# Optimization experiments

Measured on AMD Instinct MI355X. Metric: run time of the kernel, lower is better.

Reference implementation:

```python
import jax, jax.numpy as jnp
import numpy as np

N_EDGES = 320000
HIDDEN = 128
EDGE_DIM = 8


def setup_inputs() -> dict:
    key = jax.random.key(0)
    k1, k2, k3, k4 = jax.random.split(key, 4)
    h_v = jax.random.normal(k1, (N_EDGES, HIDDEN), dtype=jnp.float32)
    h_w = jax.random.normal(k2, (N_EDGES, HIDDEN), dtype=jnp.float32)
    # discrete edge types, one-hot encoded as float (as the module expects)
    edge_types = jax.random.randint(k3, (N_EDGES,), 0, EDGE_DIM)
    edge_features = jax.nn.one_hot(edge_types, EDGE_DIM, dtype=jnp.float32)
    # learned parameter: one (hidden, hidden) matrix per edge type
    edge_matrices = jax.random.normal(k4, (EDGE_DIM, HIDDEN, HIDDEN), dtype=jnp.float32) * 0.01
    return {"h_v": h_v, "h_w": h_w, "edge_features": edge_features,
            "edge_matrices": edge_matrices}


def reference(h_v, h_w, edge_features, edge_matrices):
    # Torch: A = einsum('ek,khd->ehd', edge_features, edge_matrices)  (huge E,H,H)
    #        messages = bmm(A, h_w[..., None]).squeeze(-1)
    # Same math, fused to avoid the (E,H,H) intermediate:
    # per-type matvec: y_ekh = sum_d edge_matrices[k,h,d] * h_w[e,d]
    y = jnp.einsum('ed,khd->ekh', h_w, edge_matrices)   # (E, K, H)
    # select/mix by (one-hot) edge type
    messages = jnp.einsum('ek,ekh->eh', edge_features, y)  # (E, H)
    return messages
```

## Files before the change

### kernel.cpp

```cpp
#include <hip/hip_runtime.h>
#include <hip/hip_bf16.h>


#define NEDGES 320000
#define HIDDEN 128
#define CHUNK  512

typedef __bf16 bf16x8 __attribute__((ext_vector_type(8)));
typedef float  f32x4  __attribute__((ext_vector_type(4)));

__device__ inline bf16x8 pack8(const float4 v0, const float4 v1) {
    bf16x8 p;
    p[0] = (__bf16)v0.x; p[1] = (__bf16)v0.y; p[2] = (__bf16)v0.z; p[3] = (__bf16)v0.w;
    p[4] = (__bf16)v1.x; p[5] = (__bf16)v1.y; p[6] = (__bf16)v1.z; p[7] = (__bf16)v1.w;
    return p;
}

__global__ __launch_bounds__(256, 2) void matrix_message_kernel(
    const float* __restrict__ h_w,
    const float* __restrict__ ef,
    const float* __restrict__ M,
    float*       __restrict__ out)
{
    __shared__ unsigned short list[CHUNK];
    __shared__ int cnt;
    __shared__ __align__(16) unsigned char Abuf[64 * 272];

    const int tid  = threadIdx.x;
    const int w    = tid >> 6;
    const int lane = tid & 63;
    const int q    = lane >> 4;
    const int c    = lane & 15;
    const int k    = blockIdx.y;
    const int e0   = blockIdx.x * CHUNK;

    if (tid == 0) cnt = 0;

    const float* Mb = M + (size_t)k * (HIDDEN * HIDDEN);
    bf16x8 b[2][4];
#pragma unroll
    for (int nt = 0; nt < 2; ++nt)
#pragma unroll
        for (int kk = 0; kk < 4; ++kk) {
            const int h = 32 * w + nt * 16 + c;
            const float4* s4 = (const float4*)(Mb + (size_t)h * HIDDEN + kk * 32 + q * 8);
            b[nt][kk] = pack8(s4[0], s4[1]);
        }

    __syncthreads();

#pragma unroll
    for (int t = tid; t < CHUNK; t += 256) {
        float f = ef[(size_t)(e0 + t) * 8 + k];
        if (f > 0.5f) {
            int p = atomicAdd(&cnt, 1);
            list[p] = (unsigned short)t;
        }
    }
    __syncthreads();

    const int n_g = cnt;
    for (int g = 0; g < n_g; g += 64) {
#pragma unroll
        for (int r4 = 0; r4 < 4; ++r4) {
            const int r   = r4 * 16 + (tid >> 4);
            const int idx = g + r;
            const int e_loc = list[(idx < n_g) ? idx : 0];
            const float4* src = (const float4*)(h_w + (size_t)(e0 + e_loc) * HIDDEN);
            float4 v0 = src[(tid & 15) * 2];
            float4 v1 = src[(tid & 15) * 2 + 1];
            *(bf16x8*)(Abuf + r * 272 + (tid & 15) * 16) = pack8(v0, v1);
        }
        __syncthreads();

        for (int s = 0; s < 4 && g + s * 16 < n_g; ++s) {
            bf16x8 a[4];
#pragma unroll
            for (int kk = 0; kk < 4; ++kk)
                a[kk] = *(const bf16x8*)(Abuf + (s * 16 + c) * 272 + kk * 64 + q * 16);

            f32x4 acc0 = {0.f, 0.f, 0.f, 0.f};
            f32x4 acc1 = {0.f, 0.f, 0.f, 0.f};
#pragma unroll
            for (int kk = 0; kk < 4; ++kk) {
                acc0 = __builtin_amdgcn_mfma_f32_16x16x32_bf16(a[kk], b[0][kk], acc0, 0, 0, 0);
                acc1 = __builtin_amdgcn_mfma_f32_16x16x32_bf16(a[kk], b[1][kk], acc1, 0, 0, 0);
            }

#pragma unroll
            for (int reg = 0; reg < 4; ++reg) {
                const int idx = g + s * 16 + q * 4 + reg;
                if (idx < n_g) {
                    const size_t row = (size_t)(e0 + list[idx]) * HIDDEN;
                    out[row + 32 * w + c]      = acc0[reg];
                    out[row + 32 * w + 16 + c] = acc1[reg];
                }
            }
        }
        __syncthreads();
    }
}

extern "C" void kernel_launch(void* const* d_in, const int* in_sizes, int n_in,
                              void* d_out, int out_size, void* d_ws, size_t ws_size,
                              hipStream_t stream) {
    const float* h_w = (const float*)d_in[1];
    const float* ef  = (const float*)d_in[2];
    const float* M   = (const float*)d_in[3];
    float*       out = (float*)d_out;

    dim3 grid(NEDGES / CHUNK, 8, 1);
    dim3 block(256, 1, 1);
    matrix_message_kernel<<<grid, block, 0, stream>>>(h_w, ef, M, out);
}
```

Measured before the change: 370.0 us.

## Double-buffer gathered rows, ballot-compact edge lists, and vectorize output stores

Each block now covers a larger edge chunk. The gathered h_w tile is double-buffered in LDS, with the global loads for the next 64-row group issued into registers before the MFMAs on the current group, so gather latency overlaps compute and one barrier per iteration is dropped. Edge-list compaction uses a wave ballot plus popcount with one atomic per wave instead of one per matching edge. The MFMA operands are swapped so each lane holds four consecutive hidden outputs and can write them as float4 stores. Launch bounds request higher occupancy, which risks register pressure from the prefetch registers, and larger chunks mean fewer blocks.

```diff
diff --git a/kernel.cpp b/kernel.cpp
--- a/kernel.cpp
+++ b/kernel.cpp
@@ -4,7 +4,9 @@
 
 #define NEDGES 320000
 #define HIDDEN 128
-#define CHUNK  512
+#define CHUNK  2560
+#define RSTRIDE 272
+#define HALF   (64 * RSTRIDE)
 
 typedef __bf16 bf16x8 __attribute__((ext_vector_type(8)));
 typedef float  f32x4  __attribute__((ext_vector_type(4)));
@@ -16,7 +18,7 @@
     return p;
 }
 
-__global__ __launch_bounds__(256, 2) void matrix_message_kernel(
+__global__ __launch_bounds__(256, 4) void matrix_message_kernel(
     const float* __restrict__ h_w,
     const float* __restrict__ ef,
     const float* __restrict__ M,
@@ -24,7 +26,7 @@
 {
     __shared__ unsigned short list[CHUNK];
     __shared__ int cnt;
-    __shared__ __align__(16) unsigned char Abuf[64 * 272];
+    __shared__ __align__(16) unsigned char Abuf[2][HALF];
 
     const int tid  = threadIdx.x;
     const int w    = tid >> 6;
@@ -50,54 +52,85 @@
     __syncthreads();
 
 #pragma unroll
-    for (int t = tid; t < CHUNK; t += 256) {
-        float f = ef[(size_t)(e0 + t) * 8 + k];
-        if (f > 0.5f) {
-            int p = atomicAdd(&cnt, 1);
-            list[p] = (unsigned short)t;
+    for (int t0 = 0; t0 < CHUNK; t0 += 256) {
+        const int t = t0 + tid;
+        const bool m = ef[(size_t)(e0 + t) * 8 + k] > 0.5f;
+        const unsigned long long mask = __ballot(m);
+        int base = 0;
+        if (lane == 0) base = atomicAdd(&cnt, __popcll(mask));
+        base = __shfl(base, 0);
+        if (m) {
+            const int off = __popcll(mask & ((1ull << lane) - 1ull));
+            list[base + off] = (unsigned short)t;
         }
     }
     __syncthreads();
 
     const int n_g = cnt;
+    if (n_g == 0) return;
+
+    const int rr = tid >> 4;
+    const int cc = tid & 15;
+
+    float4 p0[4], p1[4];
+#pragma unroll
+    for (int r4 = 0; r4 < 4; ++r4) {
+        const int idx = r4 * 16 + rr;
+        const int e_loc = list[(idx < n_g) ? idx : 0];
+        const float4* src = (const float4*)(h_w + (size_t)(e0 + e_loc) * HIDDEN + cc * 8);
+        p0[r4] = src[0];
+        p1[r4] = src[1];
+    }
+#pragma unroll
+    for (int r4 = 0; r4 < 4; ++r4)
+        *(bf16x8*)(&Abuf[0][(r4 * 16 + rr) * RSTRIDE + cc * 16]) = pack8(p0[r4], p1[r4]);
+
+    int cur = 0;
     for (int g = 0; g < n_g; g += 64) {
-#pragma unroll
-        for (int r4 = 0; r4 < 4; ++r4) {
-            const int r   = r4 * 16 + (tid >> 4);
-            const int idx = g + r;
-            const int e_loc = list[(idx < n_g) ? idx : 0];
-            const float4* src = (const float4*)(h_w + (size_t)(e0 + e_loc) * HIDDEN);
-            float4 v0 = src[(tid & 15) * 2];
-            float4 v1 = src[(tid & 15) * 2 + 1];
-            *(bf16x8*)(Abuf + r * 272 + (tid & 15) * 16) = pack8(v0, v1);
-        }
         __syncthreads();
 
+        const bool pf = (g + 64 < n_g);
+        if (pf) {
+#pragma unroll
+            for (int r4 = 0; r4 < 4; ++r4) {
+                const int idx = g + 64 + r4 * 16 + rr;
+                const int e_loc = list[(idx < n_g) ? idx : 0];
+                const float4* src = (const float4*)(h_w + (size_t)(e0 + e_loc) * HIDDEN + cc * 8);
+                p0[r4] = src[0];
+                p1[r4] = src[1];
+            }
+        }
+
+        const unsigned char* Ab = Abuf[cur];
         for (int s = 0; s < 4 && g + s * 16 < n_g; ++s) {
             bf16x8 a[4];
 #pragma unroll
             for (int kk = 0; kk < 4; ++kk)
-                a[kk] = *(const bf16x8*)(Abuf + (s * 16 + c) * 272 + kk * 64 + q * 16);
+                a[kk] = *(const bf16x8*)(Ab + (s * 16 + c) * RSTRIDE + kk * 64 + q * 16);
 
             f32x4 acc0 = {0.f, 0.f, 0.f, 0.f};
             f32x4 acc1 = {0.f, 0.f, 0.f, 0.f};
 #pragma unroll
             for (int kk = 0; kk < 4; ++kk) {
-                acc0 = __builtin_amdgcn_mfma_f32_16x16x32_bf16(a[kk], b[0][kk], acc0, 0, 0, 0);
-                acc1 = __builtin_amdgcn_mfma_f32_16x16x32_bf16(a[kk], b[1][kk], acc1, 0, 0, 0);
+                acc0 = __builtin_amdgcn_mfma_f32_16x16x32_bf16(b[0][kk], a[kk], acc0, 0, 0, 0);
+                acc1 = __builtin_amdgcn_mfma_f32_16x16x32_bf16(b[1][kk], a[kk], acc1, 0, 0, 0);
             }
 
-#pragma unroll
-            for (int reg = 0; reg < 4; ++reg) {
-                const int idx = g + s * 16 + q * 4 + reg;
-                if (idx < n_g) {
-                    const size_t row = (size_t)(e0 + list[idx]) * HIDDEN;
-                    out[row + 32 * w + c]      = acc0[reg];
-                    out[row + 32 * w + 16 + c] = acc1[reg];
-                }
+            const int idx = g + s * 16 + c;
+            if (idx < n_g) {
+                float* dst = out + (size_t)(e0 + list[idx]) * HIDDEN + 32 * w + q * 4;
+                *(float4*)dst        = *(const float4*)&acc0;
+                *(float4*)(dst + 16) = *(const float4*)&acc1;
             }
         }
-        __syncthreads();
+
+        if (pf) {
+            unsigned char* An = Abuf[cur ^ 1];
+#pragma unroll
+            for (int r4 = 0; r4 < 4; ++r4)
+                *(bf16x8*)(&An[(r4 * 16 + rr) * RSTRIDE + cc * 16]) = pack8(p0[r4], p1[r4]);
+        }
+        cur ^= 1;
     }
 }
 
```

New measurement: 369.5 us. About the same (-0.1%).

## Stage type matrix in LDS, swap MFMA operands, register double-buffer edge gathers

Applied to the files above, without the earlier changes.

The per-type weight matrix is now converted to bf16 once per block and kept in LDS, and the MFMA operands are swapped so each wave holds 16 gathered edge rows in registers and loops over all 128 output columns. Each wave works on its own 16-edge groups with a two-stage register double buffer that prefetches the next group's gather while computing the current one, which removes the per-group __syncthreads. Stores become float4 per row, list compaction uses a wave ballot with one atomic per wave, and the chunk size grows to 2560 with launch bounds of 4 blocks per SU. This adds per-block LDS weight staging (about 34KB) and fewer blocks in the grid, and register pressure from the two 32-float buffers may limit occupancy.

```diff
diff --git a/kernel.cpp b/kernel.cpp
--- a/kernel.cpp
+++ b/kernel.cpp
@@ -4,10 +4,13 @@
 
 #define NEDGES 320000
 #define HIDDEN 128
-#define CHUNK  512
+#define CHUNK  2560
+#define RS     272
 
 typedef __bf16 bf16x8 __attribute__((ext_vector_type(8)));
 typedef float  f32x4  __attribute__((ext_vector_type(4)));
+
+struct G { float4 v[8]; };
 
 __device__ inline bf16x8 pack8(const float4 v0, const float4 v1) {
     bf16x8 p;
@@ -16,7 +19,48 @@
     return p;
 }
 
-__global__ __launch_bounds__(256, 2) void matrix_message_kernel(
+__device__ inline void gather(const float* __restrict__ h_w,
+                              const unsigned short* list, int e0, int n_g,
+                              int base, int q, int c, G& g) {
+    int idx = base + c;
+    if (idx >= n_g) idx = n_g - 1;
+    const float* src = h_w + (size_t)(e0 + list[idx]) * HIDDEN + q * 8;
+#pragma unroll
+    for (int kk = 0; kk < 4; ++kk) {
+        g.v[2 * kk]     = *(const float4*)(src + kk * 32);
+        g.v[2 * kk + 1] = *(const float4*)(src + kk * 32 + 4);
+    }
+}
+
+__device__ inline void compute(const unsigned char* Mlds,
+                               const unsigned short* list,
+                               float* __restrict__ out, int e0, int n_g,
+                               int base, int q, int c, const G& g) {
+    bf16x8 bf[4];
+#pragma unroll
+    for (int kk = 0; kk < 4; ++kk) bf[kk] = pack8(g.v[2 * kk], g.v[2 * kk + 1]);
+
+    const int  idx = base + c;
+    const bool ok  = idx < n_g;
+    float* dst = out + (size_t)(e0 + list[ok ? idx : 0]) * HIDDEN + q * 4;
+
+#pragma unroll
+    for (int nt = 0; nt < 8; ++nt) {
+        const unsigned char* arow = Mlds + (size_t)(nt * 16 + c) * RS + q * 16;
+        bf16x8 a0 = *(const bf16x8*)(arow);
+        bf16x8 a1 = *(const bf16x8*)(arow + 64);
+        bf16x8 a2 = *(const bf16x8*)(arow + 128);
+        bf16x8 a3 = *(const bf16x8*)(arow + 192);
+        f32x4 acc = {0.f, 0.f, 0.f, 0.f};
+        acc = __builtin_amdgcn_mfma_f32_16x16x32_bf16(a0, bf[0], acc, 0, 0, 0);
+        acc = __builtin_amdgcn_mfma_f32_16x16x32_bf16(a1, bf[1], acc, 0, 0, 0);
+        acc = __builtin_amdgcn_mfma_f32_16x16x32_bf16(a2, bf[2], acc, 0, 0, 0);
+        acc = __builtin_amdgcn_mfma_f32_16x16x32_bf16(a3, bf[3], acc, 0, 0, 0);
+        if (ok) *(float4*)(dst + nt * 16) = *(const float4*)&acc;
+    }
+}
+
+__global__ __launch_bounds__(256, 4) void matrix_message_kernel(
     const float* __restrict__ h_w,
     const float* __restrict__ ef,
     const float* __restrict__ M,
@@ -24,7 +68,7 @@
 {
     __shared__ unsigned short list[CHUNK];
     __shared__ int cnt;
-    __shared__ __align__(16) unsigned char Abuf[64 * 272];
+    __shared__ __align__(16) unsigned char Mlds[128 * RS];
 
     const int tid  = threadIdx.x;
     const int w    = tid >> 6;
@@ -35,69 +79,54 @@
     const int e0   = blockIdx.x * CHUNK;
 
     if (tid == 0) cnt = 0;
+    __syncthreads();
 
     const float* Mb = M + (size_t)k * (HIDDEN * HIDDEN);
-    bf16x8 b[2][4];
 #pragma unroll
-    for (int nt = 0; nt < 2; ++nt)
-#pragma unroll
-        for (int kk = 0; kk < 4; ++kk) {
-            const int h = 32 * w + nt * 16 + c;
-            const float4* s4 = (const float4*)(Mb + (size_t)h * HIDDEN + kk * 32 + q * 8);
-            b[nt][kk] = pack8(s4[0], s4[1]);
-        }
-
-    __syncthreads();
+    for (int i = 0; i < 8; ++i) {
+        const int chunk = i * 256 + tid;
+        const int row = chunk >> 4, j = chunk & 15;
+        const float4* s4 = (const float4*)(Mb + (size_t)row * HIDDEN + j * 8);
+        float4 v0 = s4[0], v1 = s4[1];
+        *(bf16x8*)(Mlds + (size_t)row * RS + j * 16) = pack8(v0, v1);
+    }
 
 #pragma unroll
-    for (int t = tid; t < CHUNK; t += 256) {
-        float f = ef[(size_t)(e0 + t) * 8 + k];
-        if (f > 0.5f) {
-            int p = atomicAdd(&cnt, 1);
-            list[p] = (unsigned short)t;
+    for (int t0 = 0; t0 < CHUNK; t0 += 256) {
+        const int t = t0 + tid;
+        const bool m = ef[(size_t)(e0 + t) * 8 + k] > 0.5f;
+        const unsigned long long mask = __ballot(m);
+        int base = 0;
+        if (lane == 0) base = atomicAdd(&cnt, __popcll(mask));
+        base = __shfl(base, 0);
+        if (m) {
+            const int off = __popcll(mask & ((1ull << lane) - 1ull));
+            list[base + off] = (unsigned short)t;
         }
     }
     __syncthreads();
 
-    const int n_g = cnt;
-    for (int g = 0; g < n_g; g += 64) {
-#pragma unroll
-        for (int r4 = 0; r4 < 4; ++r4) {
-            const int r   = r4 * 16 + (tid >> 4);
-            const int idx = g + r;
-            const int e_loc = list[(idx < n_g) ? idx : 0];
-            const float4* src = (const float4*)(h_w + (size_t)(e0 + e_loc) * HIDDEN);
-            float4 v0 = src[(tid & 15) * 2];
-            float4 v1 = src[(tid & 15) * 2 + 1];
-            *(bf16x8*)(Abuf + r * 272 + (tid & 15) * 16) = pack8(v0, v1);
-        }
-        __syncthreads();
+    const int n_g  = cnt;
+    const int ng16 = (n_g + 15) >> 4;
+    if (w >= ng16) return;
 
-        for (int s = 0; s < 4 && g + s * 16 < n_g; ++s) {
-            bf16x8 a[4];
-#pragma unroll
-            for (int kk = 0; kk < 4; ++kk)
-                a[kk] = *(const bf16x8*)(Abuf + (s * 16 + c) * 272 + kk * 64 + q * 16);
+    G A, B;
+    int gi = w;
+    gather(h_w, list, e0, n_g, gi * 16, q, c, A);
+    while (true) {
+        const int gn = gi + 4;
+        const bool hasB = gn < ng16;
+        if (hasB) gather(h_w, list, e0, n_g, gn * 16, q, c, B);
+        compute(Mlds, list, out, e0, n_g, gi * 16, q, c, A);
+        if (!hasB) break;
+        gi = gn;
 
-            f32x4 acc0 = {0.f, 0.f, 0.f, 0.f};
-            f32x4 acc1 = {0.f, 0.f, 0.f, 0.f};
-#pragma unroll
-            for (int kk = 0; kk < 4; ++kk) {
-                acc0 = __builtin_amdgcn_mfma_f32_16x16x32_bf16(a[kk], b[0][kk], acc0, 0, 0, 0);
-                acc1 = __builtin_amdgcn_mfma_f32_16x16x32_bf16(a[kk], b[1][kk], acc1, 0, 0, 0);
-            }
-
-#pragma unroll
-            for (int reg = 0; reg < 4; ++reg) {
-                const int idx = g + s * 16 + q * 4 + reg;
-                if (idx < n_g) {
-                    const size_t row = (size_t)(e0 + list[idx]) * HIDDEN;
-                    out[row + 32 * w + c]      = acc0[reg];
-                    out[row + 32 * w + 16 + c] = acc1[reg];
-                }
-            }
-        }
-        __syncthreads();
+        const int gn2 = gi + 4;
+        const bool hasA = gn2 < ng16;
+        if (hasA) gather(h_w, list, e0, n_g, gn2 * 16, q, c, A);
+        compute(Mlds, list, out, e0, n_g, gi * 16, q, c, B);
+        if (!hasA) break;
+        gi = gn2;
     }
 }
 
```

After: 473.1 us. 27.8% more time.

## Per-wave independent tiles with register prefetch, full-matrix B, ballot compaction

Applied to the files above, without the earlier changes.

Each wave now keeps the whole 128x128 type matrix in registers and processes its own 16-edge groups independently, with no block-wide barriers in the main loop. The next group's gather is prefetched into registers while the current one is computed. Outputs are transposed through a per-wave LDS buffer so stores go out as float4 rows. List compaction switches to wave ballot plus one atomic per wave. CHUNK grows to 2560, which cuts the block count and amortizes the matrix load, but the larger register footprint risks occupancy loss or spills.

```diff
diff --git a/kernel.cpp b/kernel.cpp
--- a/kernel.cpp
+++ b/kernel.cpp
@@ -4,16 +4,75 @@
 
 #define NEDGES 320000
 #define HIDDEN 128
-#define CHUNK  512
+#define CHUNK  2560
+#define RS     272
 
 typedef __bf16 bf16x8 __attribute__((ext_vector_type(8)));
 typedef float  f32x4  __attribute__((ext_vector_type(4)));
+
+struct G { float4 v[8]; };
 
 __device__ inline bf16x8 pack8(const float4 v0, const float4 v1) {
     bf16x8 p;
     p[0] = (__bf16)v0.x; p[1] = (__bf16)v0.y; p[2] = (__bf16)v0.z; p[3] = (__bf16)v0.w;
     p[4] = (__bf16)v1.x; p[5] = (__bf16)v1.y; p[6] = (__bf16)v1.z; p[7] = (__bf16)v1.w;
     return p;
+}
+
+__device__ inline void gather(const float* __restrict__ h_w,
+                              const unsigned short* list, int e0, int n_g,
+                              int gbase, int q, int c, G& g) {
+#pragma unroll
+    for (int rb = 0; rb < 4; ++rb) {
+        int idx = gbase + rb * 4 + q;
+        if (idx >= n_g) idx = 0;
+        const float* src = h_w + (size_t)(e0 + list[idx]) * HIDDEN + c * 8;
+        g.v[2 * rb]     = *(const float4*)src;
+        g.v[2 * rb + 1] = *(const float4*)(src + 4);
+    }
+}
+
+__device__ inline void stage(unsigned char* buf, int q, int c, const G& g) {
+#pragma unroll
+    for (int rb = 0; rb < 4; ++rb)
+        *(bf16x8*)(buf + (rb * 4 + q) * RS + c * 16) = pack8(g.v[2 * rb], g.v[2 * rb + 1]);
+}
+
+__device__ inline void load_bfr(const unsigned char* buf, int q, int c, bf16x8* bfr) {
+#pragma unroll
+    for (int kk = 0; kk < 4; ++kk)
+        bfr[kk] = *(const bf16x8*)(buf + c * RS + kk * 64 + q * 16);
+}
+
+__device__ inline void mfma_dstore(const bf16x8 (&m)[8][4], unsigned char* buf,
+                                   const bf16x8* bfr, const unsigned short* list,
+                                   float* __restrict__ out, int e0, int n_g,
+                                   int gbase, int q, int c) {
+#pragma unroll
+    for (int half = 0; half < 2; ++half) {
+        f32x4 acc[4];
+#pragma unroll
+        for (int nt = 0; nt < 4; ++nt) {
+            f32x4 a = {0.f, 0.f, 0.f, 0.f};
+#pragma unroll
+            for (int kk = 0; kk < 4; ++kk)
+                a = __builtin_amdgcn_mfma_f32_16x16x32_bf16(m[half * 4 + nt][kk], bfr[kk], a, 0, 0, 0);
+            acc[nt] = a;
+        }
+#pragma unroll
+        for (int nt = 0; nt < 4; ++nt)
+            *(f32x4*)(buf + c * RS + nt * 64 + q * 16) = acc[nt];
+#pragma unroll
+        for (int rb = 0; rb < 4; ++rb) {
+            const int r = rb * 4 + q;
+            const int idx = gbase + r;
+            f32x4 d = *(const f32x4*)(buf + r * RS + c * 16);
+            if (idx < n_g) {
+                float* dst = out + (size_t)(e0 + list[idx]) * HIDDEN + half * 64 + c * 4;
+                *(float4*)dst = *(const float4*)&d;
+            }
+        }
+    }
 }
 
 __global__ __launch_bounds__(256, 2) void matrix_message_kernel(
@@ -24,7 +83,7 @@
 {
     __shared__ unsigned short list[CHUNK];
     __shared__ int cnt;
-    __shared__ __align__(16) unsigned char Abuf[64 * 272];
+    __shared__ __align__(16) unsigned char Stg[4][16 * RS];
 
     const int tid  = threadIdx.x;
     const int w    = tid >> 6;
@@ -35,69 +94,55 @@
     const int e0   = blockIdx.x * CHUNK;
 
     if (tid == 0) cnt = 0;
+    __syncthreads();
 
     const float* Mb = M + (size_t)k * (HIDDEN * HIDDEN);
-    bf16x8 b[2][4];
+    bf16x8 m[8][4];
 #pragma unroll
-    for (int nt = 0; nt < 2; ++nt)
+    for (int nt = 0; nt < 8; ++nt)
 #pragma unroll
         for (int kk = 0; kk < 4; ++kk) {
-            const int h = 32 * w + nt * 16 + c;
-            const float4* s4 = (const float4*)(Mb + (size_t)h * HIDDEN + kk * 32 + q * 8);
-            b[nt][kk] = pack8(s4[0], s4[1]);
+            const float* src = Mb + (size_t)(nt * 16 + c) * HIDDEN + kk * 32 + q * 8;
+            m[nt][kk] = pack8(*(const float4*)src, *(const float4*)(src + 4));
         }
 
-    __syncthreads();
-
 #pragma unroll
-    for (int t = tid; t < CHUNK; t += 256) {
-        float f = ef[(size_t)(e0 + t) * 8 + k];
-        if (f > 0.5f) {
-            int p = atomicAdd(&cnt, 1);
-            list[p] = (unsigned short)t;
+    for (int t0 = 0; t0 < CHUNK; t0 += 256) {
+        const int t = t0 + tid;
+        const bool mt = ef[(size_t)(e0 + t) * 8 + k] > 0.5f;
+        const unsigned long long mask = __ballot(mt);
+        int base = 0;
+        if (lane == 0) base = atomicAdd(&cnt, __popcll(mask));
+        base = __shfl(base, 0);
+        if (mt) {
+            const int off = __popcll(mask & ((1ull << lane) - 1ull));
+            list[base + off] = (unsigned short)t;
         }
     }
     __syncthreads();
 
-    const int n_g = cnt;
-    for (int g = 0; g < n_g; g += 64) {
-#pragma unroll
-        for (int r4 = 0; r4 < 4; ++r4) {
-            const int r   = r4 * 16 + (tid >> 4);
-            const int idx = g + r;
-            const int e_loc = list[(idx < n_g) ? idx : 0];
-            const float4* src = (const float4*)(h_w + (size_t)(e0 + e_loc) * HIDDEN);
-            float4 v0 = src[(tid & 15) * 2];
-            float4 v1 = src[(tid & 15) * 2 + 1];
-            *(bf16x8*)(Abuf + r * 272 + (tid & 15) * 16) = pack8(v0, v1);
-        }
-        __syncthreads();
+    const int n_g  = cnt;
+    const int ng16 = (n_g + 15) >> 4;
+    if (w >= ng16) return;
 
-        for (int s = 0; s < 4 && g + s * 16 < n_g; ++s) {
-            bf16x8 a[4];
-#pragma unroll
-            for (int kk = 0; kk < 4; ++kk)
-                a[kk] = *(const bf16x8*)(Abuf + (s * 16 + c) * 272 + kk * 64 + q * 16);
+    unsigned char* buf = Stg[w];
 
-            f32x4 acc0 = {0.f, 0.f, 0.f, 0.f};
-            f32x4 acc1 = {0.f, 0.f, 0.f, 0.f};
-#pragma unroll
-            for (int kk = 0; kk < 4; ++kk) {
-                acc0 = __builtin_amdgcn_mfma_f32_16x16x32_bf16(a[kk], b[0][kk], acc0, 0, 0, 0);
-                acc1 = __builtin_amdgcn_mfma_f32_16x16x32_bf16(a[kk], b[1][kk], acc1, 0, 0, 0);
-            }
+    G cur, nxt;
+    int gi = w;
+    gather(h_w, list, e0, n_g, gi * 16, q, c, cur);
+    bool hasn = (gi + 4) < ng16;
+    if (hasn) gather(h_w, list, e0, n_g, (gi + 4) * 16, q, c, nxt);
 
-#pragma unroll
-            for (int reg = 0; reg < 4; ++reg) {
-                const int idx = g + s * 16 + q * 4 + reg;
-                if (idx < n_g) {
-                    const size_t row = (size_t)(e0 + list[idx]) * HIDDEN;
-                    out[row + 32 * w + c]      = acc0[reg];
-                    out[row + 32 * w + 16 + c] = acc1[reg];
-                }
-            }
-        }
-        __syncthreads();
+    bf16x8 bfr[4];
+    for (;;) {
+        stage(buf, q, c, cur);
+        load_bfr(buf, q, c, bfr);
+        mfma_dstore(m, buf, bfr, list, out, e0, n_g, gi * 16, q, c);
+        if (!hasn) break;
+        gi += 4;
+        cur = nxt;
+        hasn = (gi + 4) < ng16;
+        if (hasn) gather(h_w, list, e0, n_g, (gi + 4) * 16, q, c, nxt);
     }
 }
 
```

After: 403.7 us. +9.1%, slower.
